# Performance work log

Hardware: AMD Instinct MI355X
Metric: run time of the kernel (lower is better)

## Reference

```python
import jax, jax.numpy as jnp
import numpy as np

B, LQ, LK, H = 4, 512, 512, 128


def _orthogonal(key, n, dtype=jnp.float32):
    a = jax.random.normal(key, (n, n), dtype=dtype)
    q, r = jnp.linalg.qr(a)
    return q * jnp.sign(jnp.diag(r))[None, :]


def setup_inputs() -> dict:
    key = jax.random.key(0)
    kq, kk, ku, kt, kb, kw, kwb = jax.random.split(key, 7)
    queries = jax.random.normal(kq, (B, LQ, H), dtype=jnp.float32)
    keys = jax.random.normal(kk, (B, LK, H), dtype=jnp.float32)
    U = _orthogonal(ku, H)
    T = _orthogonal(kt, H)
    b = jax.random.uniform(kb, (H,), minval=-0.1, maxval=0.1, dtype=jnp.float32)
    # nn.Linear(H, 1): weight (1, H), bias (1,); kaiming-uniform-ish init bound
    bound = 1.0 / np.sqrt(H)
    w = jax.random.uniform(kw, (H,), minval=-bound, maxval=bound, dtype=jnp.float32)
    w_bias = jax.random.uniform(kwb, (), minval=-bound, maxval=bound, dtype=jnp.float32)
    return {"queries": queries, "keys": keys, "U": U, "T": T, "b": b, "w": w, "w_bias": w_bias}


def reference(queries, keys, U, T, b, w, w_bias):
    # qU: (B, Lq, H), kT: (B, Lk, H)
    qU = jnp.einsum('bqh,hd->bqd', queries, U)
    kT = jnp.einsum('bkh,hd->bkd', keys, T)
    # broadcast sum -> (B, Lk, Lq, H), tanh, reduce with Linear(H,1)
    s = qU[:, None, :, :] + kT[:, :, None, :] + b
    scores = jnp.einsum('bkqh,h->bkq', jnp.tanh(s), w) + w_bias
    return scores.transpose(0, 2, 1)  # (B, Lq, Lk)
```

## Files before the change

### kernel.cpp

```cpp
#include <hip/hip_runtime.h>

#define B_   4
#define LQ_  512
#define LK_  512
#define H_   128

#define RPB  4
#define QPT  4
#define KTH  256

__global__ __launch_bounds__(128) void proj_kernel(
    const float* __restrict__ queries, const float* __restrict__ keys,
    const float* __restrict__ U, const float* __restrict__ T,
    const float* __restrict__ bvec,
    float* __restrict__ Q2, float* __restrict__ K2)
{
    const int side = blockIdx.y;
    const float* __restrict__ X = side ? keys : queries;
    const float* __restrict__ M = side ? T : U;
    float* __restrict__ Y       = side ? K2 : Q2;

    const int t  = threadIdx.x;
    const int r0 = blockIdx.x * RPB;

    float acc[RPB];
#pragma unroll
    for (int i = 0; i < RPB; ++i) acc[i] = 0.f;

#pragma unroll 8
    for (int d = 0; d < H_; ++d) {
        float m = M[d * H_ + t];
#pragma unroll
        for (int i = 0; i < RPB; ++i)
            acc[i] = fmaf(X[(size_t)(r0 + i) * H_ + d], m, acc[i]);
    }

    const float C = 2.8853900817779268f;
    const float bb = side ? bvec[t] : 0.f;
#pragma unroll
    for (int i = 0; i < RPB; ++i)
        Y[(size_t)(r0 + i) * H_ + t] = C * (acc[i] + bb);
}

__global__ __launch_bounds__(KTH) void score_kernel(
    const float* __restrict__ Q2, const float* __restrict__ K2,
    const float* __restrict__ w, const float* __restrict__ wb,
    float* __restrict__ out)
{
    const int b  = blockIdx.z;
    const int q0 = blockIdx.y * QPT;
    const int k  = blockIdx.x * KTH + threadIdx.x;

    const float* __restrict__ q2r = Q2 + ((size_t)b * LQ_ + q0) * H_;
    const float* __restrict__ k2r = K2 + ((size_t)b * LK_ + k) * H_;

    float acc[QPT];
#pragma unroll
    for (int i = 0; i < QPT; ++i) acc[i] = 0.f;

#pragma unroll 4
    for (int c = 0; c < H_; c += 8) {
        float4 a0 = *(const float4*)(k2r + c);
        float4 a1 = *(const float4*)(k2r + c + 4);
        float kk[8] = {a0.x, a0.y, a0.z, a0.w, a1.x, a1.y, a1.z, a1.w};
#pragma unroll
        for (int q = 0; q < QPT; ++q) {
#pragma unroll
            for (int j = 0; j < 8; ++j) {
                float tqk = q2r[q * H_ + c + j] + kk[j];
                float e   = __builtin_amdgcn_exp2f(tqk);
                float r   = __builtin_amdgcn_rcpf(e + 1.0f);
                acc[q] = fmaf(w[c + j], r, acc[q]);
            }
        }
    }

    float base = wb[0];
#pragma unroll 16
    for (int i = 0; i < H_; ++i) base += w[i];

#pragma unroll
    for (int q = 0; q < QPT; ++q)
        out[((size_t)b * LQ_ + q0 + q) * LK_ + k] = fmaf(-2.f, acc[q], base);
}

extern "C" void kernel_launch(void* const* d_in, const int* in_sizes, int n_in,
                              void* d_out, int out_size, void* d_ws, size_t ws_size,
                              hipStream_t stream)
{
    const float* queries = (const float*)d_in[0];
    const float* keys    = (const float*)d_in[1];
    const float* U       = (const float*)d_in[2];
    const float* T       = (const float*)d_in[3];
    const float* bvec    = (const float*)d_in[4];
    const float* w       = (const float*)d_in[5];
    const float* wb      = (const float*)d_in[6];
    float* out = (float*)d_out;

    float* Q2 = (float*)d_ws;
    float* K2 = Q2 + (size_t)B_ * LQ_ * H_;

    proj_kernel<<<dim3((B_ * LQ_) / RPB, 2), 128, 0, stream>>>(
        queries, keys, U, T, bvec, Q2, K2);

    score_kernel<<<dim3(LK_ / KTH, LQ_ / QPT, B_), KTH, 0, stream>>>(
        Q2, K2, w, wb, out);
}
```

Measured before the change: 103.9 us.

## Factor exp out of inner loop and batch reciprocals four-way

Uses exp2(a+b)=exp2(a)*exp2(b) so the projection kernel stores exponentiated Q and K values, removing the per-element exp from the O(L^2 H) score loop. The inner loop then merges four sigmoid terms over one common denominator, so it needs one reciprocal per four hidden elements instead of one each. The bias sum over w also moves into the projection kernel. Risks are overflow or underflow in the product of four large exponentials, which can produce inf/NaN or lose precision for large-magnitude inputs.

New measurement: 92.77 us. -10.7%, faster.

```diff
diff --git a/kernel.cpp b/kernel.cpp
--- a/kernel.cpp
+++ b/kernel.cpp
@@ -9,19 +9,27 @@
 #define QPT  4
 #define KTH  256
 
+
 __global__ __launch_bounds__(128) void proj_kernel(
     const float* __restrict__ queries, const float* __restrict__ keys,
     const float* __restrict__ U, const float* __restrict__ T,
-    const float* __restrict__ bvec,
-    float* __restrict__ Q2, float* __restrict__ K2)
+    const float* __restrict__ bvec, const float* __restrict__ w,
+    const float* __restrict__ wb,
+    float* __restrict__ Eq, float* __restrict__ Ek, float* __restrict__ base)
 {
     const int side = blockIdx.y;
     const float* __restrict__ X = side ? keys : queries;
     const float* __restrict__ M = side ? T : U;
-    float* __restrict__ Y       = side ? K2 : Q2;
+    float* __restrict__ Y       = side ? Ek : Eq;
 
     const int t  = threadIdx.x;
     const int r0 = blockIdx.x * RPB;
+
+    if (side == 1 && blockIdx.x == 0 && t == 0) {
+        float s = wb[0];
+        for (int h = 0; h < H_; ++h) s += w[h];
+        base[0] = s;
+    }
 
     float acc[RPB];
 #pragma unroll
@@ -39,46 +47,48 @@
     const float bb = side ? bvec[t] : 0.f;
 #pragma unroll
     for (int i = 0; i < RPB; ++i)
-        Y[(size_t)(r0 + i) * H_ + t] = C * (acc[i] + bb);
+        Y[(size_t)(r0 + i) * H_ + t] =
+            __builtin_amdgcn_exp2f(C * (acc[i] + bb));
 }
 
 __global__ __launch_bounds__(KTH) void score_kernel(
-    const float* __restrict__ Q2, const float* __restrict__ K2,
-    const float* __restrict__ w, const float* __restrict__ wb,
+    const float* __restrict__ Eq, const float* __restrict__ Ek,
+    const float* __restrict__ w, const float* __restrict__ base_p,
     float* __restrict__ out)
 {
     const int b  = blockIdx.z;
     const int q0 = blockIdx.y * QPT;
     const int k  = blockIdx.x * KTH + threadIdx.x;
 
-    const float* __restrict__ q2r = Q2 + ((size_t)b * LQ_ + q0) * H_;
-    const float* __restrict__ k2r = K2 + ((size_t)b * LK_ + k) * H_;
+    const float* __restrict__ eqr = Eq + ((size_t)b * LQ_ + q0) * H_;
+    const float* __restrict__ ekr = Ek + ((size_t)b * LK_ + k) * H_;
 
     float acc[QPT];
 #pragma unroll
     for (int i = 0; i < QPT; ++i) acc[i] = 0.f;
 
 #pragma unroll 4
-    for (int c = 0; c < H_; c += 8) {
-        float4 a0 = *(const float4*)(k2r + c);
-        float4 a1 = *(const float4*)(k2r + c + 4);
-        float kk[8] = {a0.x, a0.y, a0.z, a0.w, a1.x, a1.y, a1.z, a1.w};
+    for (int c = 0; c < H_; c += 4) {
+        float4 ek4 = *(const float4*)(ekr + c);
+        float w0 = w[c], w1 = w[c + 1], w2 = w[c + 2], w3 = w[c + 3];
 #pragma unroll
         for (int q = 0; q < QPT; ++q) {
-#pragma unroll
-            for (int j = 0; j < 8; ++j) {
-                float tqk = q2r[q * H_ + c + j] + kk[j];
-                float e   = __builtin_amdgcn_exp2f(tqk);
-                float r   = __builtin_amdgcn_rcpf(e + 1.0f);
-                acc[q] = fmaf(w[c + j], r, acc[q]);
-            }
+            const float* eq = eqr + q * H_ + c;
+            float x0 = fmaf(eq[0], ek4.x, 1.f);
+            float x1 = fmaf(eq[1], ek4.y, 1.f);
+            float x2 = fmaf(eq[2], ek4.z, 1.f);
+            float x3 = fmaf(eq[3], ek4.w, 1.f);
+            float d01 = x0 * x1;
+            float d23 = x2 * x3;
+            float n01 = fmaf(w1, x0, w0 * x1);
+            float n23 = fmaf(w3, x2, w2 * x3);
+            float num = fmaf(n23, d01, n01 * d23);
+            float den = d01 * d23;
+            acc[q] = fmaf(num, __builtin_amdgcn_rcpf(den), acc[q]);
         }
     }
 
-    float base = wb[0];
-#pragma unroll 16
-    for (int i = 0; i < H_; ++i) base += w[i];
-
+    const float base = base_p[0];
 #pragma unroll
     for (int q = 0; q < QPT; ++q)
         out[((size_t)b * LQ_ + q0 + q) * LK_ + k] = fmaf(-2.f, acc[q], base);
@@ -97,12 +107,13 @@
     const float* wb      = (const float*)d_in[6];
     float* out = (float*)d_out;
 
-    float* Q2 = (float*)d_ws;
-    float* K2 = Q2 + (size_t)B_ * LQ_ * H_;
+    float* Eq   = (float*)d_ws;
+    float* Ek   = Eq + (size_t)B_ * LQ_ * H_;
+    float* base = Ek + (size_t)B_ * LK_ * H_;
 
     proj_kernel<<<dim3((B_ * LQ_) / RPB, 2), 128, 0, stream>>>(
-        queries, keys, U, T, bvec, Q2, K2);
+        queries, keys, U, T, bvec, w, wb, Eq, Ek, base);
 
     score_kernel<<<dim3(LK_ / KTH, LQ_ / QPT, B_), KTH, 0, stream>>>(
-        Q2, K2, w, wb, out);
+        Eq, Ek, w, base, out);
 }
```
